# Kernel tuning notes

Measured on AMD Instinct MI355X. Metric: run time of the kernel, lower is better.

The kernel has to match this reference:

```python
import jax, jax.numpy as jnp
import numpy as np

N, G, K, D = 16, 4096, 8, 2  # agents, grid points (64x64 flattened), fiber dim, manifold dim


def setup_inputs() -> dict:
    key = jax.random.key(0)
    k0, k1, k2, k3 = jax.random.split(key, 4)
    I = jnp.eye(K, dtype=jnp.float32)
    # frames and links: identity + small perturbation (invertible, as init_twist_scale=0.05 implies)
    omega = I + 0.05 * jax.random.normal(k0, (N, G, K, K), dtype=jnp.float32)
    links = I + 0.05 * jax.random.normal(k1, (N, D, G, K, K), dtype=jnp.float32)
    mu_q = jax.random.normal(k2, (N, G, K), dtype=jnp.float32)
    A = 0.3 * jax.random.normal(k3, (N, G, K, K), dtype=jnp.float32)
    sigma_q = A @ A.swapaxes(-1, -2) + I  # SPD covariances
    return {"omega": omega, "links": links, "mu_q": mu_q, "sigma_q": sigma_q}


def reference(omega, links, mu_q, sigma_q):
    """pairwise_alignment_with_twists: E[i,j,g] = KL(q_i || Omega_ij[q_j]).

    full_transport: Omega_ij = omega_i @ V_i @ inv(omega_j),
    V_i = I + sum_d (link_{i,d} - I)   (links depend only on i, per source).
    """
    I = jnp.eye(K, dtype=omega.dtype)
    V = I + jnp.sum(links - I, axis=1)                       # (N,G,K,K)
    T = omega @ V                                            # omega_i V_i, (N,G,K,K)
    omega_inv = jnp.linalg.inv(omega)                        # (N,G,K,K)
    Om = jnp.einsum('igab,jgbc->ijgac', T, omega_inv)        # (N,N,G,K,K)

    mu_t = jnp.einsum('ijgab,jgb->ijga', Om, mu_q)           # transported means
    sig_t = jnp.einsum('ijgab,jgbc,ijgdc->ijgad', Om, sigma_q, Om)  # Om Sigma Om^T

    inv2 = jnp.linalg.inv(sig_t)                             # Sigma2^{-1}
    diff = mu_t - mu_q[:, None]                              # (N,N,G,K)
    tr = jnp.einsum('ijgab,igba->ijg', inv2, sigma_q)        # tr(Sigma2^{-1} Sigma1)
    quad = jnp.einsum('ijga,ijgab,ijgb->ijg', diff, inv2, diff)
    ld2 = jnp.linalg.slogdet(sig_t)[1]                       # (N,N,G)
    ld1 = jnp.linalg.slogdet(sigma_q)[1]                     # (N,G)
    E = 0.5 * (tr + quad - K + ld2 - ld1[:, None, :])
    # zero the diagonal (i == j skipped in the original loop)
    mask = 1.0 - jnp.eye(N, dtype=E.dtype)
    return E * mask[:, :, None]
```

## Files before the change

kernel.cpp:

```cpp
#include <hip/hip_runtime.h>
#include <math.h>

#define NN 16
#define GG 4096
#define GP 2
#define STR 68
#define NWG (GG / GP)

template <int CTRL>
__device__ __forceinline__ float dppf(float x) {
    return __builtin_bit_cast(float, __builtin_amdgcn_mov_dpp(
        __builtin_bit_cast(int, x), CTRL, 0xF, 0xF, true));
}
__device__ __forceinline__ float qb(float x, int L) {
    switch (L) {
        case 0:  return dppf<0x00>(x);
        case 1:  return dppf<0x55>(x);
        case 2:  return dppf<0xAA>(x);
        default: return dppf<0xFF>(x);
    }
}
__device__ __forceinline__ float qsum(float x) {
    x += dppf<0xB1>(x);
    x += dppf<0x4E>(x);
    return x;
}
__device__ __forceinline__ void bcast_row(float out[8], const float r0[8],
                                          const float r1[8], int k) {
#pragma unroll
    for (int c = 0; c < 8; ++c) {
        float s = (k < 4) ? r0[c] : r1[c];
        out[c] = qb(s, k & 3);
    }
}
__device__ __forceinline__ float sel_lo(const float r[8], int q) {
    return (q == 0) ? r[0] : (q == 1) ? r[1] : (q == 2) ? r[2] : r[3];
}
__device__ __forceinline__ float sel_hi(const float r[8], int q) {
    return (q == 0) ? r[4] : (q == 1) ? r[5] : (q == 2) ? r[6] : r[7];
}
__device__ __forceinline__ void ld_row(float r[8], const float* p) {
    float4 x = *(const float4*)p, y = *(const float4*)(p + 4);
    r[0] = x.x; r[1] = x.y; r[2] = x.z; r[3] = x.w;
    r[4] = y.x; r[5] = y.y; r[6] = y.z; r[7] = y.w;
}
__device__ __forceinline__ void st_row(float* p, const float r[8]) {
    *(float4*)p       = make_float4(r[0], r[1], r[2], r[3]);
    *(float4*)(p + 4) = make_float4(r[4], r[5], r[6], r[7]);
}
__device__ __forceinline__ float dot8(const float a[8], const float b[8]) {
    float s = a[0] * b[0];
    s = fmaf(a[1], b[1], s); s = fmaf(a[2], b[2], s);
    s = fmaf(a[3], b[3], s); s = fmaf(a[4], b[4], s);
    s = fmaf(a[5], b[5], s); s = fmaf(a[6], b[6], s);
    s = fmaf(a[7], b[7], s);
    return s;
}

__device__ __forceinline__ float gj4(float r0[8], float r1[8], int q) {
    float pp = 1.0f;
#pragma unroll
    for (int k = 0; k < 8; ++k) {
        float Mk[8];
        bcast_row(Mk, r0, r1, k);
        float p = Mk[k];
        pp *= p;
        float ip = 1.0f / p;
        bool own0 = (k < 4) && (q == k);
        bool own1 = (k >= 4) && (q == k - 4);
        float m0 = -(own0 ? -1.0f : r0[k]) * ip;
        float m1 = -(own1 ? -1.0f : r1[k]) * ip;
#pragma unroll
        for (int c = 0; c < 8; ++c) {
            float b0 = own0 ? 0.0f : r0[c];
            float b1 = own1 ? 0.0f : r1[c];
            r0[c] = fmaf(m0, Mk[c], b0);
            r1[c] = fmaf(m1, Mk[c], b1);
        }
        r0[k] = m0;
        r1[k] = m1;
    }
    return pp;
}

__global__ __launch_bounds__(256) void pairkl_kernel(
    const float* __restrict__ omega, const float* __restrict__ links,
    const float* __restrict__ mu, const float* __restrict__ sigma,
    float* __restrict__ out) {
    __shared__ __align__(16) float sh_om[GP][NN][STR];
    __shared__ __align__(16) float sh_sg[GP][NN][STR];
    __shared__ __align__(16) float sh_wv[GP][NN][STR];
    __shared__ __align__(16) float sh_mu[GP][NN][8];
    __shared__ __align__(16) float sh_u [GP][NN][8];
    __shared__ __align__(16) float sh_w [GP][NN][8];
    __shared__ __align__(16) float sh_sc[GP][NN][4];

    const int bid  = blockIdx.x;
    const int work = (bid & 7) * (NWG / 8) + (bid >> 3);
    const int g0   = work * GP;
    const int t    = threadIdx.x;

    {
        const int gl = t >> 7, s = t & 127;
        const int g  = g0 + gl;
        const float4* om4 = (const float4*)omega;
        const float4* sg4 = (const float4*)sigma;
        const float4* lk4 = (const float4*)links;
#pragma unroll
        for (int k = 0; k < 2; ++k) {
            int fc = s + 128 * k;
            int i = fc >> 4, qq = fc & 15;
            int b4 = (i * GG + g) * 16 + qq;
            float4 o  = om4[b4];
            float4 sv = sg4[b4];
            float4 l0 = lk4[((i * 2 + 0) * GG + g) * 16 + qq];
            float4 l1 = lk4[((i * 2 + 1) * GG + g) * 16 + qq];
            float4 v = make_float4(l0.x + l1.x, l0.y + l1.y, l0.z + l1.z, l0.w + l1.w);
            int e0 = qq * 4;
            if (((e0 + 0) >> 3) == ((e0 + 0) & 7)) v.x -= 1.f;
            if (((e0 + 1) >> 3) == ((e0 + 1) & 7)) v.y -= 1.f;
            if (((e0 + 2) >> 3) == ((e0 + 2) & 7)) v.z -= 1.f;
            if (((e0 + 3) >> 3) == ((e0 + 3) & 7)) v.w -= 1.f;
            *(float4*)&sh_om[gl][i][e0] = o;
            *(float4*)&sh_sg[gl][i][e0] = sv;
            *(float4*)&sh_wv[gl][i][e0] = v;
        }
        if (t < 64) {
            int gl2 = t >> 5, mi = (t >> 1) & 15, h = t & 1;
            const float4* mu4 = (const float4*)mu;
            *(float4*)&sh_mu[gl2][mi][h * 4] = mu4[(mi * GG + g0 + gl2) * 2 + h];
        }
    }
    __syncthreads();

    const int wid  = t >> 6;
    const int gl   = wid & 1;
    const int isB  = wid >> 1;
    const int lane = t & 63;
    const int item = lane >> 2;
    const int q    = lane & 3;

    float R0[8], R1[8];
    float mq[8];
    ld_row(mq, &sh_mu[gl][item][0]);

    if (!isB) {
        float o0[8], o1[8];
        ld_row(o0, &sh_om[gl][item][q * 8]);
        ld_row(o1, &sh_om[gl][item][(q + 4) * 8]);
#pragma unroll
        for (int c = 0; c < 8; ++c) { R0[c] = 0.f; R1[c] = 0.f; }
        const float* vv = &sh_wv[gl][item][0];
#pragma unroll
        for (int b = 0; b < 8; ++b) {
            float vr[8]; ld_row(vr, vv + b * 8);
#pragma unroll
            for (int c = 0; c < 8; ++c) {
                R0[c] = fmaf(o0[b], vr[c], R0[c]);
                R1[c] = fmaf(o1[b], vr[c], R1[c]);
            }
        }
        float ppT = gj4(R0, R1, q);
        if (q == 0) sh_sc[gl][item][0] = 2.0f * logf(fabsf(ppT));
    } else {
        float a0[8], a1[8];
        ld_row(a0, &sh_om[gl][item][q * 8]);
        ld_row(a1, &sh_om[gl][item][(q + 4) * 8]);
        float ppo = gj4(a0, a1, q);
        ld_row(R0, &sh_sg[gl][item][q * 8]);
        ld_row(R1, &sh_sg[gl][item][(q + 4) * 8]);
        float pps = gj4(R0, R1, q);
        float cq = dot8(R0, mq) * sel_lo(mq, q) + dot8(R1, mq) * sel_hi(mq, q);
        float cc = qsum(cq);
        if (q == 0) {
            sh_sc[gl][item][1] = 2.0f * logf(fabsf(ppo));
            sh_sc[gl][item][2] = logf(fabsf(pps));
            sh_sc[gl][item][3] = cc;
        }
    }
    __syncthreads();

    if (!isB) {
        float Z0[8], Z1[8];
#pragma unroll
        for (int c = 0; c < 8; ++c) { Z0[c] = 0.f; Z1[c] = 0.f; }
        const float* sg = &sh_sg[gl][item][0];
#pragma unroll
        for (int b = 0; b < 8; ++b) {
            float sr[8]; ld_row(sr, sg + b * 8);
#pragma unroll
            for (int c = 0; c < 8; ++c) {
                Z0[c] = fmaf(R0[b], sr[c], Z0[c]);
                Z1[c] = fmaf(R1[b], sr[c], Z1[c]);
            }
        }
        float Q0[8], Q1[8];
#pragma unroll
        for (int c = 0; c < 8; ++c) {
            float Wc[8]; bcast_row(Wc, R0, R1, c);
            Q0[c] = dot8(Z0, Wc);
            Q1[c] = dot8(Z1, Wc);
        }
        st_row(&sh_wv[gl][item][q * 8], Q0);
        st_row(&sh_wv[gl][item][(q + 4) * 8], Q1);
        sh_u[gl][item][q]     = dot8(R0, mq);
        sh_u[gl][item][q + 4] = dot8(R1, mq);
    } else {
        float S0[8], S1[8], oq[8], oq4[8];
#pragma unroll
        for (int c = 0; c < 8; ++c) { S0[c] = 0.f; S1[c] = 0.f; }
        const float* om = &sh_om[gl][item][0];
#pragma unroll
        for (int b = 0; b < 8; ++b) {
            float orow[8]; ld_row(orow, om + b * 8);
#pragma unroll
            for (int c = 0; c < 8; ++c) {
                S0[c] = fmaf(R0[b], orow[c], S0[c]);
                S1[c] = fmaf(R1[b], orow[c], S1[c]);
            }
            oq[b]  = sel_lo(orow, q);
            oq4[b] = sel_hi(orow, q);
        }
        float P0[8], P1[8];
#pragma unroll
        for (int c = 0; c < 8; ++c) { P0[c] = 0.f; P1[c] = 0.f; }
#pragma unroll
        for (int a = 0; a < 8; ++a) {
            float Sa[8]; bcast_row(Sa, S0, S1, a);
#pragma unroll
            for (int c = 0; c < 8; ++c) {
                P0[c] = fmaf(oq[a],  Sa[c], P0[c]);
                P1[c] = fmaf(oq4[a], Sa[c], P1[c]);
            }
        }
        float wp[8];
        {
            float mlo = sel_lo(mq, q), mhi = sel_hi(mq, q);
#pragma unroll
            for (int c = 0; c < 8; ++c)
                wp[c] = qsum(fmaf(mlo, S0[c], mhi * S1[c]));
        }
        st_row(&sh_om[gl][item][q * 8], P0);
        st_row(&sh_om[gl][item][(q + 4) * 8], P1);
        if (q == 0) st_row(&sh_w[gl][item][0], wp);
    }
    __syncthreads();

    {
        const int gl2 = t >> 7, r2 = t & 127;
        const int i2 = r2 >> 3, jb = r2 & 7;
        const int j0 = jb, j1 = jb + 8;
        const float* Qp = &sh_wv[gl2][i2][0];
        const float* Pa = &sh_om[gl2][j0][0];
        const float* Pb = &sh_om[gl2][j1][0];
        float u[8]; ld_row(u, &sh_u[gl2][i2][0]);
        float tr0 = 0.f, tr1 = 0.f, up0 = 0.f, up1 = 0.f;
#pragma unroll
        for (int a = 0; a < 8; ++a) {
            float qr[8]; ld_row(qr, Qp + a * 8);
            float p0[8]; ld_row(p0, Pa + a * 8);
            float p1[8]; ld_row(p1, Pb + a * 8);
            float s0 = 0.f, s1 = 0.f;
#pragma unroll
            for (int c = 0; c < 8; ++c) {
                tr0 = fmaf(p0[c], qr[c], tr0);
                tr1 = fmaf(p1[c], qr[c], tr1);
                s0  = fmaf(p0[c], u[c], s0);
                s1  = fmaf(p1[c], u[c], s1);
            }
            up0 = fmaf(u[a], s0, up0);
            up1 = fmaf(u[a], s1, up1);
        }
        float w0[8]; ld_row(w0, &sh_w[gl2][j0][0]);
        float w1[8]; ld_row(w1, &sh_w[gl2][j1][0]);
        float wu0 = dot8(w0, u), wu1 = dot8(w1, u);
        float4 sci = *(const float4*)&sh_sc[gl2][i2][0];
        float4 sj0 = *(const float4*)&sh_sc[gl2][j0][0];
        float4 sj1 = *(const float4*)&sh_sc[gl2][j1][0];
        float ai  = sci.x - sci.z;
        float s0j = sj0.z - sj0.y + sj0.w - 8.0f;
        float s1j = sj1.z - sj1.y + sj1.w - 8.0f;
        float E0 = 0.5f * (tr0 + up0 - 2.f * wu0 + ai + s0j);
        float E1 = 0.5f * (tr1 + up1 - 2.f * wu1 + ai + s1j);
        int g = g0 + gl2;
        out[(i2 * NN + j0) * GG + g] = (i2 == j0) ? 0.f : E0;
        out[(i2 * NN + j1) * GG + g] = (i2 == j1) ? 0.f : E1;
    }
}

extern "C" void kernel_launch(void* const* d_in, const int* in_sizes, int n_in,
                              void* d_out, int out_size, void* d_ws, size_t ws_size,
                              hipStream_t stream) {
    const float* omega = (const float*)d_in[0];
    const float* links = (const float*)d_in[1];
    const float* mu    = (const float*)d_in[2];
    const float* sigma = (const float*)d_in[3];
    float* out = (float*)d_out;
    hipLaunchKernelGGL(pairkl_kernel, dim3(NWG), dim3(256), 0, stream,
                       omega, links, mu, sigma, out);
}
```

Before: 29.67 us.

## Fold pairwise KL terms into a single augmented dot product with 2x2 register tiling

Each row of the i-side and j-side shared tiles is augmented with the mean vector, the linear coefficients and the scalar log-det and constant terms. The final pairwise stage then becomes one 76-length dot product per (i,j) pair, computed with float4 loads over a 2x2 register tile by 128 threads. This removes the separate u, w and scalar shared arrays and cuts shared-memory reads per output. In exchange the row stride grows, half the threads sit idle in the last stage, and the summation order changes, so floating-point results can differ slightly.

```diff
diff --git a/kernel.cpp b/kernel.cpp
--- a/kernel.cpp
+++ b/kernel.cpp
@@ -4,7 +4,7 @@
 #define NN 16
 #define GG 4096
 #define GP 2
-#define STR 68
+#define STR 76
 #define NWG (GG / GP)
 
 template <int CTRL>
@@ -91,9 +91,9 @@
     __shared__ __align__(16) float sh_sg[GP][NN][STR];
     __shared__ __align__(16) float sh_wv[GP][NN][STR];
     __shared__ __align__(16) float sh_mu[GP][NN][8];
-    __shared__ __align__(16) float sh_u [GP][NN][8];
-    __shared__ __align__(16) float sh_w [GP][NN][8];
-    __shared__ __align__(16) float sh_sc[GP][NN][4];
+    __shared__ float sh_ld1[GP][NN];
+#define sh_x sh_wv
+#define sh_y sh_om
 
     const int bid  = blockIdx.x;
     const int work = (bid & 7) * (NWG / 8) + (bid >> 3);
@@ -144,6 +144,8 @@
     float mq[8];
     ld_row(mq, &sh_mu[gl][item][0]);
 
+    float ldT = 0.f, ld1B = 0.f, ldoB = 0.f, ccB = 0.f;
+
     if (!isB) {
         float o0[8], o1[8];
         ld_row(o0, &sh_om[gl][item][q * 8]);
@@ -161,7 +163,7 @@
             }
         }
         float ppT = gj4(R0, R1, q);
-        if (q == 0) sh_sc[gl][item][0] = 2.0f * logf(fabsf(ppT));
+        ldT = logf(fabsf(ppT));
     } else {
         float a0[8], a1[8];
         ld_row(a0, &sh_om[gl][item][q * 8]);
@@ -171,16 +173,18 @@
         ld_row(R1, &sh_sg[gl][item][(q + 4) * 8]);
         float pps = gj4(R0, R1, q);
         float cq = dot8(R0, mq) * sel_lo(mq, q) + dot8(R1, mq) * sel_hi(mq, q);
-        float cc = qsum(cq);
-        if (q == 0) {
-            sh_sc[gl][item][1] = 2.0f * logf(fabsf(ppo));
-            sh_sc[gl][item][2] = logf(fabsf(pps));
-            sh_sc[gl][item][3] = cc;
-        }
+        ccB  = qsum(cq);
+        ld1B = logf(fabsf(pps));
+        ldoB = logf(fabsf(ppo));
+        if (q == 0) sh_ld1[gl][item] = ld1B;
     }
     __syncthreads();
 
     if (!isB) {
+        float u_lo = dot8(R0, mq), u_hi = dot8(R1, mq);
+        float uf[8];
+#pragma unroll
+        for (int c = 0; c < 4; ++c) { uf[c] = qb(u_lo, c); uf[c + 4] = qb(u_hi, c); }
         float Z0[8], Z1[8];
 #pragma unroll
         for (int c = 0; c < 8; ++c) { Z0[c] = 0.f; Z1[c] = 0.f; }
@@ -194,17 +198,22 @@
                 Z1[c] = fmaf(R1[b], sr[c], Z1[c]);
             }
         }
-        float Q0[8], Q1[8];
+        float X0[8], X1[8];
 #pragma unroll
         for (int c = 0; c < 8; ++c) {
             float Wc[8]; bcast_row(Wc, R0, R1, c);
-            Q0[c] = dot8(Z0, Wc);
-            Q1[c] = dot8(Z1, Wc);
-        }
-        st_row(&sh_wv[gl][item][q * 8], Q0);
-        st_row(&sh_wv[gl][item][(q + 4) * 8], Q1);
-        sh_u[gl][item][q]     = dot8(R0, mq);
-        sh_u[gl][item][q + 4] = dot8(R1, mq);
+            X0[c] = fmaf(u_lo, uf[c], dot8(Z0, Wc));
+            X1[c] = fmaf(u_hi, uf[c], dot8(Z1, Wc));
+        }
+        st_row(&sh_x[gl][item][q * 8], X0);
+        st_row(&sh_x[gl][item][(q + 4) * 8], X1);
+        if (q == 0) {
+            float ld1 = sh_ld1[gl][item];
+            float a_i = 2.f * ldT - ld1;
+            *(float4*)&sh_x[gl][item][64] = make_float4(uf[0], uf[1], uf[2], uf[3]);
+            *(float4*)&sh_x[gl][item][68] = make_float4(uf[4], uf[5], uf[6], uf[7]);
+            *(float4*)&sh_x[gl][item][72] = make_float4(a_i, 1.f, 0.f, 0.f);
+        }
     } else {
         float S0[8], S1[8], oq[8], oq4[8];
 #pragma unroll
@@ -240,51 +249,46 @@
             for (int c = 0; c < 8; ++c)
                 wp[c] = qsum(fmaf(mlo, S0[c], mhi * S1[c]));
         }
-        st_row(&sh_om[gl][item][q * 8], P0);
-        st_row(&sh_om[gl][item][(q + 4) * 8], P1);
-        if (q == 0) st_row(&sh_w[gl][item][0], wp);
+        st_row(&sh_y[gl][item][q * 8], P0);
+        st_row(&sh_y[gl][item][(q + 4) * 8], P1);
+        if (q == 0) {
+            float s_j = ld1B - 2.f * ldoB + ccB - 8.0f;
+            *(float4*)&sh_y[gl][item][64] =
+                make_float4(-2.f * wp[0], -2.f * wp[1], -2.f * wp[2], -2.f * wp[3]);
+            *(float4*)&sh_y[gl][item][68] =
+                make_float4(-2.f * wp[4], -2.f * wp[5], -2.f * wp[6], -2.f * wp[7]);
+            *(float4*)&sh_y[gl][item][72] = make_float4(1.f, s_j, 0.f, 0.f);
+        }
     }
     __syncthreads();
 
-    {
-        const int gl2 = t >> 7, r2 = t & 127;
-        const int i2 = r2 >> 3, jb = r2 & 7;
-        const int j0 = jb, j1 = jb + 8;
-        const float* Qp = &sh_wv[gl2][i2][0];
-        const float* Pa = &sh_om[gl2][j0][0];
-        const float* Pb = &sh_om[gl2][j1][0];
-        float u[8]; ld_row(u, &sh_u[gl2][i2][0]);
-        float tr0 = 0.f, tr1 = 0.f, up0 = 0.f, up1 = 0.f;
-#pragma unroll
-        for (int a = 0; a < 8; ++a) {
-            float qr[8]; ld_row(qr, Qp + a * 8);
-            float p0[8]; ld_row(p0, Pa + a * 8);
-            float p1[8]; ld_row(p1, Pb + a * 8);
-            float s0 = 0.f, s1 = 0.f;
-#pragma unroll
-            for (int c = 0; c < 8; ++c) {
-                tr0 = fmaf(p0[c], qr[c], tr0);
-                tr1 = fmaf(p1[c], qr[c], tr1);
-                s0  = fmaf(p0[c], u[c], s0);
-                s1  = fmaf(p1[c], u[c], s1);
-            }
-            up0 = fmaf(u[a], s0, up0);
-            up1 = fmaf(u[a], s1, up1);
-        }
-        float w0[8]; ld_row(w0, &sh_w[gl2][j0][0]);
-        float w1[8]; ld_row(w1, &sh_w[gl2][j1][0]);
-        float wu0 = dot8(w0, u), wu1 = dot8(w1, u);
-        float4 sci = *(const float4*)&sh_sc[gl2][i2][0];
-        float4 sj0 = *(const float4*)&sh_sc[gl2][j0][0];
-        float4 sj1 = *(const float4*)&sh_sc[gl2][j1][0];
-        float ai  = sci.x - sci.z;
-        float s0j = sj0.z - sj0.y + sj0.w - 8.0f;
-        float s1j = sj1.z - sj1.y + sj1.w - 8.0f;
-        float E0 = 0.5f * (tr0 + up0 - 2.f * wu0 + ai + s0j);
-        float E1 = 0.5f * (tr1 + up1 - 2.f * wu1 + ai + s1j);
-        int g = g0 + gl2;
-        out[(i2 * NN + j0) * GG + g] = (i2 == j0) ? 0.f : E0;
-        out[(i2 * NN + j1) * GG + g] = (i2 == j1) ? 0.f : E1;
+    if (t < 128) {
+        const int gl2 = t >> 6, r = t & 63;
+        const int i0 = r >> 3, j0 = r & 7;
+        const int i1 = i0 + 8, j1 = j0 + 8;
+        const float4* x0 = (const float4*)&sh_x[gl2][i0][0];
+        const float4* x1 = (const float4*)&sh_x[gl2][i1][0];
+        const float4* y0 = (const float4*)&sh_y[gl2][j0][0];
+        const float4* y1 = (const float4*)&sh_y[gl2][j1][0];
+        float d00 = 0.f, d01 = 0.f, d10 = 0.f, d11 = 0.f;
+#pragma unroll
+        for (int k = 0; k < STR / 4; ++k) {
+            float4 a0 = x0[k], a1 = x1[k], b0 = y0[k], b1 = y1[k];
+            d00 = fmaf(a0.x, b0.x, d00); d00 = fmaf(a0.y, b0.y, d00);
+            d00 = fmaf(a0.z, b0.z, d00); d00 = fmaf(a0.w, b0.w, d00);
+            d01 = fmaf(a0.x, b1.x, d01); d01 = fmaf(a0.y, b1.y, d01);
+            d01 = fmaf(a0.z, b1.z, d01); d01 = fmaf(a0.w, b1.w, d01);
+            d10 = fmaf(a1.x, b0.x, d10); d10 = fmaf(a1.y, b0.y, d10);
+            d10 = fmaf(a1.z, b0.z, d10); d10 = fmaf(a1.w, b0.w, d10);
+            d11 = fmaf(a1.x, b1.x, d11); d11 = fmaf(a1.y, b1.y, d11);
+            d11 = fmaf(a1.z, b1.z, d11); d11 = fmaf(a1.w, b1.w, d11);
+        }
+        const int g = g0 + gl2;
+        const bool dg = (i0 == j0);
+        out[(i0 * NN + j0) * GG + g] = dg ? 0.f : 0.5f * d00;
+        out[(i0 * NN + j1) * GG + g] = 0.5f * d01;
+        out[(i1 * NN + j0) * GG + g] = 0.5f * d10;
+        out[(i1 * NN + j1) * GG + g] = dg ? 0.f : 0.5f * d11;
     }
 }
 
```

New measurement: 29.53 us. No clear change (-0.5%).
